# Kernel optimization log

Hardware: AMD Instinct MI355X
Metric: run time of the kernel (lower is better)

Reference implementation:

```python
import jax, jax.numpy as jnp
import numpy as np

B, TXT_T, MEL_T, N_MEL = 8, 200, 800, 80
PAD_MAG = 1.0e12


def setup_inputs() -> dict:
    key = jax.random.key(0)
    k1, k2, k3, k4 = jax.random.split(key, 4)
    mu_logvar = jax.random.normal(k1, (B, TXT_T, 2 * N_MEL), dtype=jnp.float32)
    melspec = jax.random.normal(k2, (B, N_MEL, MEL_T), dtype=jnp.float32)
    # lengths are 1-based (indexed as length-1), keep them in [T//2, T]
    text_lengths = jax.random.randint(k3, (B,), TXT_T // 2, TXT_T + 1)
    mel_lengths = jax.random.randint(k4, (B,), MEL_T // 2, MEL_T + 1)
    return {
        "mu_logvar": mu_logvar,
        "melspec": melspec,
        "text_lengths": text_lengths,
        "mel_lengths": mel_lengths,
    }


def _log_prob_matrix(mu_logvar, melspec):
    # melspec: [B, n_mel, mel_T] -> x: [B, 1, mel_T, n_mel]
    x = jnp.transpose(melspec, (0, 2, 1))[:, None, :, :]
    mu = mu_logvar[:, :, :N_MEL][:, :, None, :]       # [B, txt_T, 1, n_mel]
    logvar = mu_logvar[:, :, N_MEL:][:, :, None, :]   # [B, txt_T, 1, n_mel]
    # -0.5 * mean_over_mel( (x-mu)^2 / exp(logvar) + logvar )
    sq = (x - mu) ** 2
    return (-0.5 * (sq * jnp.exp(-logvar) + logvar)).mean(axis=3)  # [B, txt_T, mel_T]


def reference(mu_logvar, melspec, text_lengths, mel_lengths):
    lp = _log_prob_matrix(mu_logvar, melspec)  # [B, txt_T, mel_T]

    # log_alpha column carry, with a leading pad row (index 0 stays -PAD_MAG)
    init = jnp.full((B, TXT_T + 1), -PAD_MAG, dtype=lp.dtype)
    init = init.at[:, 1].set(lp[:, 0, 0])

    def step(a, lp_t):  # a: [B, txt_T+1], lp_t: [B, txt_T]
        # logsumexp over {stay, advance}; original adds 1e-7 to prev values
        new_rows = jnp.logaddexp(a[:, 1:] + 1e-7, a[:, :-1] + 1e-7) + lp_t
        a = a.at[:, 1:].set(new_rows)
        return a, new_rows

    lp_rest = jnp.moveaxis(lp[:, :, 1:], 2, 0)  # [mel_T-1, B, txt_T]
    _, cols = jax.lax.scan(step, init, lp_rest)  # cols: [mel_T-1, B, txt_T]

    log_alpha = jnp.concatenate(
        [init[:, 1:, None], jnp.moveaxis(cols, 0, 2)], axis=2
    )  # [B, txt_T, mel_T]

    b = jnp.arange(B)
    alpha_last = log_alpha[b, text_lengths - 1, mel_lengths - 1]
    alpha_last = alpha_last / mel_lengths.astype(alpha_last.dtype)
    mdn_loss = -alpha_last.mean()
    return mdn_loss, lp
```

## Files before the change

### kernel.cpp

```cpp
#include <hip/hip_runtime.h>
#include <math.h>

#define BB 8
#define TXT_T 200
#define MEL_T 800
#define N_MEL 80
#define NTHR 192
#define CSTR 1024
#define LOG2E 1.44269504088896340736f
#define LN2   0.69314718055994530942f
#define EPS2  (1e-7f * LOG2E)
#define NPAD  -1.0e12f

__device__ __forceinline__ float exp2_hw(float x) {
#if __has_builtin(__builtin_amdgcn_exp2f)
    return __builtin_amdgcn_exp2f(x);
#else
    return __expf(LN2 * x);
#endif
}

__device__ __forceinline__ float lse2(float A, float B) {
    float m = fmaxf(A, B);
    float e = exp2_hw(-fabsf(A - B));
    return m + __log2f(1.0f + e);
}

template <int D>
__device__ __forceinline__ float dpp_shr(float v, float old) {
#if __has_builtin(__builtin_amdgcn_update_dpp)
    return __int_as_float(__builtin_amdgcn_update_dpp(
        __float_as_int(old), __float_as_int(v), 0x110 | D, 0xF, 0xF, false));
#else
    float t = __shfl_up(v, D);
    return ((threadIdx.x & 15) < D) ? old : t;
#endif
}

__global__ void __launch_bounds__(256) lp_kernel(
        const float* __restrict__ mu_logvar,
        const float* __restrict__ melspec,
        float* __restrict__ out_lp,
        float* __restrict__ lpT) {
    const int bt = blockIdx.x;
    const int b  = bt / TXT_T;
    const int tid = threadIdx.x;

    __shared__ float s_mu[N_MEL];
    __shared__ float s_ev[N_MEL];
    __shared__ float s_lv[N_MEL];
    __shared__ float s_sumlv;

    if (tid < N_MEL) {
        float mu = mu_logvar[(size_t)bt * (2 * N_MEL) + tid];
        float lv = mu_logvar[(size_t)bt * (2 * N_MEL) + N_MEL + tid];
        s_mu[tid] = mu;
        s_ev[tid] = __expf(-lv);
        s_lv[tid] = lv;
    }
    __syncthreads();
    if (tid == 0) {
        float s = 0.f;
        #pragma unroll
        for (int n = 0; n < N_MEL; ++n) s += s_lv[n];
        s_sumlv = s;
    }
    __syncthreads();

    if (tid < MEL_T / 4) {
        const float4* ms4 = (const float4*)(melspec + (size_t)b * N_MEL * MEL_T);
        float ax = 0.f, ay = 0.f, az = 0.f, aw = 0.f;
        #pragma unroll 8
        for (int n = 0; n < N_MEL; ++n) {
            float4 x = ms4[(size_t)n * (MEL_T / 4) + tid];
            float mu = s_mu[n];
            float ev = s_ev[n];
            float d0 = x.x - mu; ax += d0 * d0 * ev;
            float d1 = x.y - mu; ay += d1 * d1 * ev;
            float d2 = x.z - mu; az += d2 * d2 * ev;
            float d3 = x.w - mu; aw += d3 * d3 * ev;
        }
        const float c = -0.5f / (float)N_MEL;
        float slv = s_sumlv;
        float l0 = c * (ax + slv);
        float l1 = c * (ay + slv);
        float l2 = c * (az + slv);
        float l3 = c * (aw + slv);

        size_t ob = (size_t)bt * MEL_T + tid * 4;
        out_lp[ob + 0] = l0;
        out_lp[ob + 1] = l1;
        out_lp[ob + 2] = l2;
        out_lp[ob + 3] = l3;

        float4 v;
        v.x = l0 * LOG2E + EPS2;
        v.y = l1 * LOG2E + EPS2;
        v.z = l2 * LOG2E + EPS2;
        v.w = l3 * LOG2E + EPS2;
        *(float4*)(lpT + (size_t)bt * CSTR + tid * 4) = v;
    } else {
        float4 zz; zz.x = 0.f; zz.y = 0.f; zz.z = 0.f; zz.w = 0.f;
        *(float4*)(lpT + (size_t)bt * CSTR + 800 + (tid - 200) * 4) = zz;
    }
}

__device__ __forceinline__ void stage_col(const float* row, float* sb,
                                          int w, int lane) {
    __builtin_amdgcn_global_load_lds(
        (const __attribute__((address_space(1))) void*)(row + w * 256 + lane * 4),
        (__attribute__((address_space(3))) void*)(sb + w * 256),
        16, 0, 0);
}

__global__ void __launch_bounds__(NTHR) scan_kernel(
        const float* __restrict__ lpT,
        const int* __restrict__ text_lengths,
        const int* __restrict__ mel_lengths,
        float* __restrict__ alpha_out) {
    __shared__ float sbuf[2][784];
    __shared__ float tot[2][4][2];
    const int b = blockIdx.x;
    const int tid = threadIdx.x;
    const int w = tid >> 6;
    const int lane = tid & 63;

    const int melL1 = mel_lengths[b] - 1;
    const int txtL1 = text_lengths[b] - 1;
    const float scale = LN2 / (float)(melL1 + 1);
    const int estar = melL1 - txtL1;
    const int gtid = estar >> 2;
    const int gk = estar & 3;

    const float* cb = lpT + (size_t)b * TXT_T * CSTR;

    if (tid < 16) { sbuf[0][768 + tid] = 0.0f; sbuf[1][768 + tid] = 0.0f; }
    asm volatile("s_waitcnt lgkmcnt(0)" ::: "memory");

    float A0 = (tid == 0) ? -EPS2 : NPAD;
    float A1 = NPAD, A2 = NPAD, A3 = NPAD;

    stage_col(cb, &sbuf[0][0], w, lane);
    stage_col(cb + (size_t)1 * CSTR + 0, &sbuf[1][0], w, lane);

    int par = 0;
    for (int j = 0; j <= txtL1; ++j) {
        asm volatile("s_waitcnt vmcnt(1)" ::: "memory");
        __builtin_amdgcn_sched_barrier(0);
        asm volatile("s_barrier" ::: "memory");

        const float* sb = &sbuf[par][0];
        const int off = (j & 3) + 4 * tid;
        float al0 = sb[off + 0];
        float al1 = sb[off + 1];
        float al2 = sb[off + 2];
        float al3 = sb[off + 3];

        float be0 = al0 + A0;
        float be1 = al1 + A1;
        float be2 = al2 + A2;
        float be3 = al3 + A3;

        float I0a = al0,        I0b = be0;
        float I1a = al1 + I0a,  I1b = lse2(al1 + I0b, be1);
        float t23a = al3 + al2, t23b = lse2(al3 + be2, be3);
        float I2a = al2 + I1a,  I2b = lse2(al2 + I1b, be2);
        float I3a = t23a + I1a, I3b = lse2(t23a + I1b, t23b);

        float Ta = I3a, Tb = I3b;
        {
            float ia, ib;
            ia = dpp_shr<1>(Ta, 0.0f); ib = dpp_shr<1>(Tb, NPAD);
            Tb = lse2(Ta + ib, Tb); Ta = Ta + ia;
            ia = dpp_shr<2>(Ta, 0.0f); ib = dpp_shr<2>(Tb, NPAD);
            Tb = lse2(Ta + ib, Tb); Ta = Ta + ia;
            ia = dpp_shr<4>(Ta, 0.0f); ib = dpp_shr<4>(Tb, NPAD);
            Tb = lse2(Ta + ib, Tb); Ta = Ta + ia;
            ia = dpp_shr<8>(Ta, 0.0f); ib = dpp_shr<8>(Tb, NPAD);
            Tb = lse2(Ta + ib, Tb); Ta = Ta + ia;
        }

        float t0a = __shfl(Ta, 15), t0b = __shfl(Tb, 15);
        float t1a = __shfl(Ta, 31), t1b = __shfl(Tb, 31);
        float t2a = __shfl(Ta, 47), t2b = __shfl(Tb, 47);
        float c2a = t1a + t0a, c2b = lse2(t1a + t0b, t1b);
        float c3a = t2a + c2a, c3b = lse2(t2a + c2b, t2b);
        int row_ = lane >> 4;
        float Xa = 0.0f, Xb = NPAD;
        if (row_ == 1) { Xa = t0a; Xb = t0b; }
        if (row_ == 2) { Xa = c2a; Xb = c2b; }
        if (row_ == 3) { Xa = c3a; Xb = c3b; }
        float Fa = Ta + Xa;
        float Fb = lse2(Ta + Xb, Tb);

        float pfa = __shfl_up(Fa, 1);
        float pfb = __shfl_up(Fb, 1);
        if (lane == 63) { tot[par][w][0] = Fa; tot[par][w][1] = Fb; }
        asm volatile("s_waitcnt lgkmcnt(0)" ::: "memory");
        asm volatile("s_barrier" ::: "memory");

        {
            int jn = j + 2; if (jn > txtL1) jn = txtL1;
            stage_col(cb + (size_t)jn * CSTR + (jn & ~3), &sbuf[par][0],
                      w, lane);
        }

        float Wxa = 0.0f, Wxb = NPAD;
        if (w >= 1) { Wxa = tot[par][0][0]; Wxb = tot[par][0][1]; }
        if (w >= 2) {
            float ga = tot[par][1][0], gb = tot[par][1][1];
            Wxb = lse2(ga + Wxb, gb);
            Wxa = ga + Wxa;
        }

        float Exb;
        if (lane == 0) Exb = Wxb;
        else           Exb = lse2(pfa + Wxb, pfb);

        float B0 = lse2(I0a + Exb, I0b);
        float B1 = lse2(I1a + Exb, I1b);
        float B2 = lse2(I2a + Exb, I2b);
        float B3 = lse2(I3a + Exb, I3b);

        if (j == txtL1 && tid == gtid) {
            float g = B0;
            if (gk == 1) g = B1;
            if (gk == 2) g = B2;
            if (gk == 3) g = B3;
            alpha_out[b] = g * scale;
        }

        A0 = B0; A1 = B1; A2 = B2; A3 = B3;
        par ^= 1;
    }
    asm volatile("s_waitcnt vmcnt(0)" ::: "memory");
}

__global__ void finish_kernel(const float* __restrict__ alpha,
                              float* __restrict__ out) {
    float s = 0.f;
    #pragma unroll
    for (int b = 0; b < BB; ++b) s += alpha[b];
    out[0] = -(s / (float)BB);
}

extern "C" void kernel_launch(void* const* d_in, const int* in_sizes, int n_in,
                              void* d_out, int out_size, void* d_ws, size_t ws_size,
                              hipStream_t stream) {
    const float* mu_logvar    = (const float*)d_in[0];
    const float* melspec      = (const float*)d_in[1];
    const int*   text_lengths = (const int*)d_in[2];
    const int*   mel_lengths  = (const int*)d_in[3];
    float* out = (float*)d_out;

    float* alpha = (float*)d_ws;
    float* lpT   = (float*)d_ws + 64;

    lp_kernel<<<BB * TXT_T, 256, 0, stream>>>(mu_logvar, melspec, out + 1, lpT);
    scan_kernel<<<BB, NTHR, 0, stream>>>(lpT, text_lengths, mel_lengths, alpha);
    finish_kernel<<<1, 1, 0, stream>>>(alpha, out);
}
```

Measured before the change: 142.8 us.

## Triple-buffer scan columns and flatten log-semiring prefix with multi-way logsumexp

Reworks the sequential scan kernel. Column staging becomes triple-buffered with strided 4-byte LDS loads, so each thread reads its four values conflict-free and prefetches the next column before the compute. The per-step barrier count drops from two to one. The intra-row DPP prefix scan goes from four dependent lse2 stages to two lse4 stages, and the final cross-wave combine is folded into lse4 calls. This shortens the serial dependency chain per column in exchange for more exp2 evaluations and more outstanding memory operations.

```diff
diff --git a/kernel.cpp b/kernel.cpp
--- a/kernel.cpp
+++ b/kernel.cpp
@@ -24,6 +24,16 @@
     float m = fmaxf(A, B);
     float e = exp2_hw(-fabsf(A - B));
     return m + __log2f(1.0f + e);
+}
+__device__ __forceinline__ float lse3(float A, float B, float C) {
+    float m = fmaxf(fmaxf(A, B), C);
+    float e = exp2_hw(A - m) + exp2_hw(B - m) + exp2_hw(C - m);
+    return m + __log2f(e);
+}
+__device__ __forceinline__ float lse4(float A, float B, float C, float D) {
+    float m = fmaxf(fmaxf(A, B), fmaxf(C, D));
+    float e = exp2_hw(A - m) + exp2_hw(B - m) + exp2_hw(C - m) + exp2_hw(D - m);
+    return m + __log2f(e);
 }
 
 template <int D>
@@ -105,12 +115,16 @@
     }
 }
 
-__device__ __forceinline__ void stage_col(const float* row, float* sb,
+__device__ __forceinline__ void stage_col(const float* colbase, float* sb,
                                           int w, int lane) {
-    __builtin_amdgcn_global_load_lds(
-        (const __attribute__((address_space(1))) void*)(row + w * 256 + lane * 4),
-        (__attribute__((address_space(3))) void*)(sb + w * 256),
-        16, 0, 0);
+    #pragma unroll
+    for (int k = 0; k < 4; ++k) {
+        __builtin_amdgcn_global_load_lds(
+            (const __attribute__((address_space(1))) void*)
+                (colbase + 4 * (w * 64 + lane) + k),
+            (__attribute__((address_space(3))) void*)(sb + k * 192 + w * 64),
+            4, 0, 0);
+    }
 }
 
 __global__ void __launch_bounds__(NTHR) scan_kernel(
@@ -118,7 +132,7 @@
         const int* __restrict__ text_lengths,
         const int* __restrict__ mel_lengths,
         float* __restrict__ alpha_out) {
-    __shared__ float sbuf[2][784];
+    __shared__ float sbuf[3][768];
     __shared__ float tot[2][4][2];
     const int b = blockIdx.x;
     const int tid = threadIdx.x;
@@ -134,28 +148,23 @@
 
     const float* cb = lpT + (size_t)b * TXT_T * CSTR;
 
-    if (tid < 16) { sbuf[0][768 + tid] = 0.0f; sbuf[1][768 + tid] = 0.0f; }
-    asm volatile("s_waitcnt lgkmcnt(0)" ::: "memory");
-
     float A0 = (tid == 0) ? -EPS2 : NPAD;
     float A1 = NPAD, A2 = NPAD, A3 = NPAD;
 
-    stage_col(cb, &sbuf[0][0], w, lane);
-    stage_col(cb + (size_t)1 * CSTR + 0, &sbuf[1][0], w, lane);
+    stage_col(cb,                   &sbuf[0][0], w, lane);
+    stage_col(cb + (size_t)1 * CSTR, &sbuf[1][0], w, lane);
+    stage_col(cb + (size_t)2 * CSTR, &sbuf[2][0], w, lane);
+    asm volatile("s_waitcnt vmcnt(8)" ::: "memory");
+    __builtin_amdgcn_sched_barrier(0);
+    asm volatile("s_barrier" ::: "memory");
+
+    float al0 = sbuf[0][0 * 192 + tid];
+    float al1 = sbuf[0][1 * 192 + tid];
+    float al2 = sbuf[0][2 * 192 + tid];
+    float al3 = sbuf[0][3 * 192 + tid];
 
     int par = 0;
     for (int j = 0; j <= txtL1; ++j) {
-        asm volatile("s_waitcnt vmcnt(1)" ::: "memory");
-        __builtin_amdgcn_sched_barrier(0);
-        asm volatile("s_barrier" ::: "memory");
-
-        const float* sb = &sbuf[par][0];
-        const int off = (j & 3) + 4 * tid;
-        float al0 = sb[off + 0];
-        float al1 = sb[off + 1];
-        float al2 = sb[off + 2];
-        float al3 = sb[off + 3];
-
         float be0 = al0 + A0;
         float be1 = al1 + A1;
         float be2 = al2 + A2;
@@ -169,22 +178,30 @@
 
         float Ta = I3a, Tb = I3b;
         {
-            float ia, ib;
-            ia = dpp_shr<1>(Ta, 0.0f); ib = dpp_shr<1>(Tb, NPAD);
-            Tb = lse2(Ta + ib, Tb); Ta = Ta + ia;
-            ia = dpp_shr<2>(Ta, 0.0f); ib = dpp_shr<2>(Tb, NPAD);
-            Tb = lse2(Ta + ib, Tb); Ta = Ta + ia;
-            ia = dpp_shr<4>(Ta, 0.0f); ib = dpp_shr<4>(Tb, NPAD);
-            Tb = lse2(Ta + ib, Tb); Ta = Ta + ia;
-            ia = dpp_shr<8>(Ta, 0.0f); ib = dpp_shr<8>(Tb, NPAD);
-            Tb = lse2(Ta + ib, Tb); Ta = Ta + ia;
+            float a1 = dpp_shr<1>(Ta, 0.0f), b1 = dpp_shr<1>(Tb, NPAD);
+            float a2 = dpp_shr<2>(Ta, 0.0f), b2 = dpp_shr<2>(Tb, NPAD);
+            float a3 = dpp_shr<3>(Ta, 0.0f), b3 = dpp_shr<3>(Tb, NPAD);
+            float s1 = Ta + a1;
+            float s2 = s1 + a2;
+            Tb = lse4(Tb, Ta + b1, s1 + b2, s2 + b3);
+            Ta = s2 + a3;
+        }
+        {
+            float a4 = dpp_shr<4>(Ta, 0.0f),  b4 = dpp_shr<4>(Tb, NPAD);
+            float a8 = dpp_shr<8>(Ta, 0.0f),  b8 = dpp_shr<8>(Tb, NPAD);
+            float a12 = dpp_shr<12>(Ta, 0.0f), b12 = dpp_shr<12>(Tb, NPAD);
+            float s4 = Ta + a4;
+            float s8 = s4 + a8;
+            Tb = lse4(Tb, Ta + b4, s4 + b8, s8 + b12);
+            Ta = s8 + a12;
         }
 
         float t0a = __shfl(Ta, 15), t0b = __shfl(Tb, 15);
         float t1a = __shfl(Ta, 31), t1b = __shfl(Tb, 31);
         float t2a = __shfl(Ta, 47), t2b = __shfl(Tb, 47);
         float c2a = t1a + t0a, c2b = lse2(t1a + t0b, t1b);
-        float c3a = t2a + c2a, c3b = lse2(t2a + c2b, t2b);
+        float c3a = t2a + c2a;
+        float c3b = lse3(t2a + t1a + t0b, t2a + t1b, t2b);
         int row_ = lane >> 4;
         float Xa = 0.0f, Xb = NPAD;
         if (row_ == 1) { Xa = t0a; Xb = t0b; }
@@ -193,34 +210,35 @@
         float Fa = Ta + Xa;
         float Fb = lse2(Ta + Xb, Tb);
 
-        float pfa = __shfl_up(Fa, 1);
-        float pfb = __shfl_up(Fb, 1);
+        float pfa = dpp_shr<1>(Fa, 0.0f);
+        float pfb = dpp_shr<1>(Fb, NPAD);
+        if ((lane & 15) == 0) { pfa = Xa; pfb = Xb; }
+
         if (lane == 63) { tot[par][w][0] = Fa; tot[par][w][1] = Fb; }
-        asm volatile("s_waitcnt lgkmcnt(0)" ::: "memory");
+        asm volatile("s_waitcnt vmcnt(4) lgkmcnt(0)" ::: "memory");
+        __builtin_amdgcn_sched_barrier(0);
         asm volatile("s_barrier" ::: "memory");
 
         {
-            int jn = j + 2; if (jn > txtL1) jn = txtL1;
-            stage_col(cb + (size_t)jn * CSTR + (jn & ~3), &sbuf[par][0],
-                      w, lane);
-        }
-
-        float Wxa = 0.0f, Wxb = NPAD;
-        if (w >= 1) { Wxa = tot[par][0][0]; Wxb = tot[par][0][1]; }
-        if (w >= 2) {
-            float ga = tot[par][1][0], gb = tot[par][1][1];
-            Wxb = lse2(ga + Wxb, gb);
-            Wxa = ga + Wxa;
-        }
-
-        float Exb;
-        if (lane == 0) Exb = Wxb;
-        else           Exb = lse2(pfa + Wxb, pfb);
-
-        float B0 = lse2(I0a + Exb, I0b);
-        float B1 = lse2(I1a + Exb, I1b);
-        float B2 = lse2(I2a + Exb, I2b);
-        float B3 = lse2(I3a + Exb, I3b);
+            int jn = j + 3; if (jn > txtL1) jn = txtL1;
+            stage_col(cb + (size_t)jn * CSTR, &sbuf[j % 3][0], w, lane);
+        }
+
+        const float* sbn = &sbuf[(j + 1) % 3][0];
+        float an0 = sbn[0 * 192 + tid];
+        float an1 = sbn[1 * 192 + tid];
+        float an2 = sbn[2 * 192 + tid];
+        float an3 = sbn[3 * 192 + tid];
+
+        float Wb1 = NPAD, Wb2 = NPAD;
+        if (w == 1) { Wb1 = tot[par][0][1]; }
+        if (w == 2) { Wb1 = tot[par][1][0] + tot[par][0][1];
+                      Wb2 = tot[par][1][1]; }
+        float pa1 = pfa + Wb1, pa2 = pfa + Wb2;
+        float B0 = lse4(I0a + pa1, I0a + pa2, I0a + pfb, I0b);
+        float B1 = lse4(I1a + pa1, I1a + pa2, I1a + pfb, I1b);
+        float B2 = lse4(I2a + pa1, I2a + pa2, I2a + pfb, I2b);
+        float B3 = lse4(I3a + pa1, I3a + pa2, I3a + pfb, I3b);
 
         if (j == txtL1 && tid == gtid) {
             float g = B0;
@@ -231,6 +249,7 @@
         }
 
         A0 = B0; A1 = B1; A2 = B2; A3 = B3;
+        al0 = an0; al1 = an1; al2 = an2; al3 = an3;
         par ^= 1;
     }
     asm volatile("s_waitcnt vmcnt(0)" ::: "memory");
```

Result: slower. 202.8 us (+42.1%).
